# Kernel optimization log

Hardware: AMD Instinct MI355X
Metric: run time of the kernel (lower is better)

Reference implementation:

```python
import jax, jax.numpy as jnp
import numpy as np

B, S, D, H, E, F = 32, 196, 768, 12, 8, 3072  # batch, seq, d_model, heads, experts, ffn
DH = D // H
EPS = 1e-5


def setup_inputs() -> dict:
    key = jax.random.key(0)
    ks = jax.random.split(key, 16)
    n = lambda k, shape, s=0.02: (jax.random.normal(k, shape, dtype=jnp.float32) * s)
    return {
        "q": jax.random.normal(ks[0], (B, S, D), dtype=jnp.float32),
        "k": jax.random.normal(ks[1], (B, S, D), dtype=jnp.float32),
        "v": jax.random.normal(ks[2], (B, S, D), dtype=jnp.float32),
        "Wq": n(ks[3], (D, D)), "bq": jnp.zeros((D,), jnp.float32),
        "Wk": n(ks[4], (D, D)), "bk": jnp.zeros((D,), jnp.float32),
        "Wv": n(ks[5], (D, D)), "bv": jnp.zeros((D,), jnp.float32),
        "Wo": n(ks[6], (D, D)), "bo": jnp.zeros((D,), jnp.float32),
        "ln1_g": jnp.ones((D,), jnp.float32), "ln1_b": jnp.zeros((D,), jnp.float32),
        "ln2_g": jnp.ones((D,), jnp.float32), "ln2_b": jnp.zeros((D,), jnp.float32),
        "Wg": n(ks[7], (D, E)), "bg": jnp.zeros((E,), jnp.float32),
        "W1": n(ks[8], (E, D, F)), "b1": jnp.zeros((E, F), jnp.float32),
        "W2": n(ks[9], (E, F, D)), "b2": jnp.zeros((E, D), jnp.float32),
    }


def _layernorm(x, g, b):
    mu = jnp.mean(x, axis=-1, keepdims=True)
    var = jnp.mean(jnp.square(x - mu), axis=-1, keepdims=True)
    return (x - mu) * jax.lax.rsqrt(var + EPS) * g + b


def reference(q, k, v, Wq, bq, Wk, bk, Wv, bv, Wo, bo,
              ln1_g, ln1_b, ln2_g, ln2_b, Wg, bg, W1, b1, W2, b2):
    # --- multi-head attention (batch_first, scaled dot product) ---
    qh = (q @ Wq + bq).reshape(B, S, H, DH)
    kh = (k @ Wk + bk).reshape(B, S, H, DH)
    vh = (v @ Wv + bv).reshape(B, S, H, DH)
    scores = jnp.einsum('bqhd,bkhd->bhqk', qh, kh) / np.float32(np.sqrt(DH))
    attn = jax.nn.softmax(scores, axis=-1)
    ctx = jnp.einsum('bhqk,bkhd->bqhd', attn, vh).reshape(B, S, D)
    attn_out = ctx @ Wo + bo

    # --- residual + LN 1 ---
    x = _layernorm(q + attn_out, ln1_g, ln1_b)

    # --- MoE: per-token soft gating over per-expert FFNs ---
    gates = jax.nn.softmax(x @ Wg + bg, axis=-1)                 # [B,S,E]
    h = jax.nn.gelu(jnp.einsum('bsd,edf->bsef', x, W1) + b1,
                    approximate=False)                            # [B,S,E,F]
    y = jnp.einsum('bsef,efd->bsed', h, W2) + b2                 # [B,S,E,D]
    moe_out = jnp.einsum('bse,bsed->bsd', gates, y)              # [B,S,D]

    # --- residual + LN 2 ---
    return _layernorm(x + moe_out, ln2_g, ln2_b)
```

## Files before the change

kernel.cpp:

```cpp
#include <hip/hip_runtime.h>
#include <cmath>

#define B_  32
#define S_  196
#define D_  768
#define H_  12
#define E_  8
#define F_  3072
#define DH_ 64
#define T_  (B_ * S_)

typedef unsigned short ushort_t;
typedef short   s16x8   __attribute__((ext_vector_type(8)));
typedef __bf16  bf16x8_t __attribute__((ext_vector_type(8)));
typedef float   f32x4   __attribute__((ext_vector_type(4)));

struct ABFrag {
    unsigned int r[4];
    __device__ operator s16x8()    const { return __builtin_bit_cast(s16x8, *this); }
    __device__ operator bf16x8_t() const { return __builtin_bit_cast(bf16x8_t, *this); }
};

__device__ __forceinline__ ushort_t f2bf(float f) {
    unsigned int x = __float_as_uint(f);
    return (ushort_t)((x + 0x7fffu + ((x >> 16) & 1u)) >> 16);
}

__device__ __forceinline__ void glds16(const void* g, void* l) {
    __builtin_amdgcn_global_load_lds((const __attribute__((address_space(1))) void*)g,
                                     (__attribute__((address_space(3))) void*)l,
                                     16, 0, 0);
}

template<int EPI>
__global__ __launch_bounds__(256)
void gemm_bt(const ushort_t* __restrict__ A, const ushort_t* __restrict__ Bt,
             const float* __restrict__ bias,
             float* __restrict__ Cf, ushort_t* __restrict__ Cb,
             int M, int N, int K,
             const float* __restrict__ gates, int expert)
{
    __shared__ ushort_t Alds[128 * 32];
    __shared__ ushort_t Blds[128 * 32];

    const int tid = threadIdx.x;
    const int w  = tid >> 6, l = tid & 63;
    const int wr = w >> 1,  wc = w & 1;
    const int rg = l >> 4,  fr = l & 15;
    const int brow = blockIdx.y * 128;
    const int bcol = blockIdx.x * 128;

    const int srow = tid >> 2;
    const int scol = (tid & 3) << 3;
    const ushort_t* gA = A  + (size_t)(brow + srow) * K + scol;
    const ushort_t* gB = Bt + (size_t)(bcol + srow) * K + scol;
    ushort_t* lA = &Alds[w * 512];
    ushort_t* lB = &Blds[w * 512];

    f32x4 acc[4][4] = {};

    const int aoff = (wr * 64 + fr) * 32 + rg * 8;
    const int boff = (wc * 64 + fr) * 32 + rg * 8;

    for (int k0 = 0; k0 < K; k0 += 32) {
        if (k0) __syncthreads();
        glds16(gA,                  lA);
        glds16(gA + (size_t)64 * K, lA + 2048);
        glds16(gB,                  lB);
        glds16(gB + (size_t)64 * K, lB + 2048);
        gA += 32; gB += 32;
        __syncthreads();

        ABFrag af[4], bf[4];
        #pragma unroll
        for (int m = 0; m < 4; ++m) af[m] = *(const ABFrag*)&Alds[aoff + m * 512];
        #pragma unroll
        for (int n = 0; n < 4; ++n) bf[n] = *(const ABFrag*)&Blds[boff + n * 512];
        #pragma unroll
        for (int m = 0; m < 4; ++m)
            #pragma unroll
            for (int n = 0; n < 4; ++n)
                acc[m][n] = __builtin_amdgcn_mfma_f32_16x16x32_bf16(
                                af[m], bf[n], acc[m][n], 0, 0, 0);
    }

    #pragma unroll
    for (int m = 0; m < 4; ++m) {
        #pragma unroll
        for (int n = 0; n < 4; ++n) {
            const int col = bcol + wc * 64 + n * 16 + fr;
            const float bv = bias[col];
            #pragma unroll
            for (int j = 0; j < 4; ++j) {
                const int row = brow + wr * 64 + m * 16 + rg * 4 + j;
                float vv = acc[m][n][j] + bv;
                if (EPI == 0) {
                    Cf[(size_t)row * N + col] = vv;
                } else if (EPI == 1) {
                    vv = 0.5f * vv * (1.0f + erff(vv * 0.70710678118654752f));
                    Cb[(size_t)row * N + col] = f2bf(vv);
                } else {
                    Cf[(size_t)row * N + col] +=
                        gates[(size_t)row * E_ + expert] * vv;
                }
            }
        }
    }
}

__global__ __launch_bounds__(256)
void convert_bf16(const float* __restrict__ in, ushort_t* __restrict__ out)
{
    const int i = blockIdx.x * 256 + threadIdx.x;
    float4 v = ((const float4*)in)[i];
    ushort4 o;
    o.x = f2bf(v.x); o.y = f2bf(v.y); o.z = f2bf(v.z); o.w = f2bf(v.w);
    ((ushort4*)out)[i] = o;
}

__global__ __launch_bounds__(256)
void transpose_to_bf16(const float* __restrict__ in, ushort_t* __restrict__ out,
                       int R, int C)
{
    __shared__ float tile[64][65];
    const int bc = blockIdx.x * 64;
    const int br = blockIdx.y * 64;
    const int lr = threadIdx.x >> 4;
    const int lc = (threadIdx.x & 15) << 2;
    #pragma unroll
    for (int i = 0; i < 64; i += 16) {
        float4 v = *(const float4*)&in[(size_t)(br + lr + i) * C + bc + lc];
        tile[lr + i][lc + 0] = v.x; tile[lr + i][lc + 1] = v.y;
        tile[lr + i][lc + 2] = v.z; tile[lr + i][lc + 3] = v.w;
    }
    __syncthreads();
    #pragma unroll
    for (int i = 0; i < 64; i += 16) {
        const int orow = lr + i;
        ushort4 o;
        o.x = f2bf(tile[lc + 0][orow]);
        o.y = f2bf(tile[lc + 1][orow]);
        o.z = f2bf(tile[lc + 2][orow]);
        o.w = f2bf(tile[lc + 3][orow]);
        *(ushort4*)&out[(size_t)(bc + orow) * R + br + lc] = o;
    }
}

__global__ __launch_bounds__(256)
void attn_kernel(const float* __restrict__ qh, const float* __restrict__ kh,
                 const float* __restrict__ vh, float* __restrict__ ctx,
                 float* __restrict__ scratch)
{
    __shared__ float Ks[S_ * DH_];
    const int bh = blockIdx.x;
    const int b  = bh / H_;
    const int h  = bh % H_;
    const int tid = threadIdx.x;

    for (int idx = tid; idx < S_ * DH_; idx += 256) {
        const int s = idx >> 6, d = idx & 63;
        Ks[idx] = kh[((size_t)(b * S_ + s)) * D_ + h * DH_ + d];
    }
    __syncthreads();
    if (tid >= S_) return;

    float qf[DH_];
    const float* qrow = qh + ((size_t)(b * S_ + tid)) * D_ + h * DH_;
    #pragma unroll
    for (int d4 = 0; d4 < 16; ++d4) {
        float4 v4 = *(const float4*)(qrow + d4 * 4);
        qf[d4*4+0] = v4.x; qf[d4*4+1] = v4.y; qf[d4*4+2] = v4.z; qf[d4*4+3] = v4.w;
    }

    float* sc = scratch + (size_t)bh * (S_ * S_) + tid;
    float m = -1e30f;
    for (int k = 0; k < S_; ++k) {
        const float* kr = &Ks[k * DH_];
        float s0 = 0.f, s1 = 0.f, s2 = 0.f, s3 = 0.f;
        #pragma unroll
        for (int d = 0; d < DH_; d += 4) {
            s0 = fmaf(qf[d+0], kr[d+0], s0);
            s1 = fmaf(qf[d+1], kr[d+1], s1);
            s2 = fmaf(qf[d+2], kr[d+2], s2);
            s3 = fmaf(qf[d+3], kr[d+3], s3);
        }
        const float sv = (s0 + s1 + s2 + s3) * 0.125f;
        sc[(size_t)k * S_] = sv;
        m = fmaxf(m, sv);
    }
    float l = 0.f;
    for (int k = 0; k < S_; ++k) {
        const float p = expf(sc[(size_t)k * S_] - m);
        sc[(size_t)k * S_] = p;
        l += p;
    }
    float acc[DH_];
    #pragma unroll
    for (int d = 0; d < DH_; ++d) acc[d] = 0.f;
    const float* vbase = vh + ((size_t)b * S_) * D_ + h * DH_;
    for (int k = 0; k < S_; ++k) {
        const float p = sc[(size_t)k * S_];
        const float* vr = vbase + (size_t)k * D_;
        #pragma unroll
        for (int d4 = 0; d4 < 16; ++d4) {
            float4 v4 = *(const float4*)(vr + d4 * 4);
            acc[d4*4+0] = fmaf(p, v4.x, acc[d4*4+0]);
            acc[d4*4+1] = fmaf(p, v4.y, acc[d4*4+1]);
            acc[d4*4+2] = fmaf(p, v4.z, acc[d4*4+2]);
            acc[d4*4+3] = fmaf(p, v4.w, acc[d4*4+3]);
        }
    }
    const float inv = 1.f / l;
    float* crow = ctx + ((size_t)(b * S_ + tid)) * D_ + h * DH_;
    #pragma unroll
    for (int d = 0; d < DH_; ++d) crow[d] = acc[d] * inv;
}

__device__ __forceinline__ float block_sum(float v, float* red)
{
    __syncthreads();
    const int lane = threadIdx.x & 63;
    const int wid  = threadIdx.x >> 6;
    #pragma unroll
    for (int off = 32; off > 0; off >>= 1) v += __shfl_down(v, off);
    if (lane == 0) red[wid] = v;
    __syncthreads();
    return red[0] + red[1] + red[2] + red[3];
}

__global__ __launch_bounds__(256)
void ln_kernel(const float* __restrict__ a, const float* __restrict__ bres,
               const float* __restrict__ g, const float* __restrict__ beta,
               float* __restrict__ out)
{
    __shared__ float red[4];
    const int t   = blockIdx.x;
    const int tid = threadIdx.x;
    const float* ar = a    + (size_t)t * D_;
    const float* br = bres + (size_t)t * D_;

    float vals[3];
    float s = 0.f;
    #pragma unroll
    for (int i = 0; i < 3; ++i) {
        const int d = tid + i * 256;
        const float x = ar[d] + br[d];
        vals[i] = x;
        s += x;
    }
    s = block_sum(s, red);
    const float mu = s * (1.f / D_);
    float qv = 0.f;
    #pragma unroll
    for (int i = 0; i < 3; ++i) { const float dv = vals[i] - mu; qv += dv * dv; }
    qv = block_sum(qv, red);
    const float rstd = rsqrtf(qv * (1.f / D_) + 1e-5f);
    #pragma unroll
    for (int i = 0; i < 3; ++i) {
        const int d = tid + i * 256;
        out[(size_t)t * D_ + d] = (vals[i] - mu) * rstd * g[d] + beta[d];
    }
}

__global__ __launch_bounds__(256)
void gate_kernel(const float* __restrict__ x, const float* __restrict__ Wg,
                 const float* __restrict__ bg, float* __restrict__ gates)
{
    const int lane = threadIdx.x & 63;
    const int wid  = threadIdx.x >> 6;
    const int t = blockIdx.x * 4 + wid;
    const float* xr = x + (size_t)t * D_;

    float accv[E_];
    #pragma unroll
    for (int e = 0; e < E_; ++e) accv[e] = 0.f;
    for (int d = lane; d < D_; d += 64) {
        const float xv = xr[d];
        const float* wr = Wg + (size_t)d * E_;
        #pragma unroll
        for (int e = 0; e < E_; ++e) accv[e] = fmaf(xv, wr[e], accv[e]);
    }
    #pragma unroll
    for (int e = 0; e < E_; ++e) {
        #pragma unroll
        for (int off = 32; off > 0; off >>= 1)
            accv[e] += __shfl_down(accv[e], off);
    }
    if (lane == 0) {
        float mx = -1e30f;
        #pragma unroll
        for (int e = 0; e < E_; ++e) { accv[e] += bg[e]; mx = fmaxf(mx, accv[e]); }
        float l = 0.f;
        #pragma unroll
        for (int e = 0; e < E_; ++e) { const float p = expf(accv[e] - mx); accv[e] = p; l += p; }
        const float inv = 1.f / l;
        #pragma unroll
        for (int e = 0; e < E_; ++e) gates[(size_t)t * E_ + e] = accv[e] * inv;
    }
}

__global__ void zero_kernel(float* __restrict__ p, int n)
{
    const int i = blockIdx.x * blockDim.x + threadIdx.x;
    if (i < n) p[i] = 0.f;
}

extern "C" void kernel_launch(void* const* d_in, const int* in_sizes, int n_in,
                              void* d_out, int out_size, void* d_ws, size_t ws_size,
                              hipStream_t stream)
{
    const float* q    = (const float*)d_in[0];
    const float* k    = (const float*)d_in[1];
    const float* v    = (const float*)d_in[2];
    const float* Wq   = (const float*)d_in[3];
    const float* bq   = (const float*)d_in[4];
    const float* Wk   = (const float*)d_in[5];
    const float* bk   = (const float*)d_in[6];
    const float* Wv   = (const float*)d_in[7];
    const float* bv   = (const float*)d_in[8];
    const float* Wo   = (const float*)d_in[9];
    const float* bo   = (const float*)d_in[10];
    const float* ln1g = (const float*)d_in[11];
    const float* ln1b = (const float*)d_in[12];
    const float* ln2g = (const float*)d_in[13];
    const float* ln2b = (const float*)d_in[14];
    const float* Wg   = (const float*)d_in[15];
    const float* bg   = (const float*)d_in[16];
    const float* W1   = (const float*)d_in[17];
    const float* b1   = (const float*)d_in[18];
    const float* W2   = (const float*)d_in[19];
    const float* b2   = (const float*)d_in[20];
    float* out = (float*)d_out;
    float* ws  = (float*)d_ws;

    const size_t TD = (size_t)T_ * D_;
    const size_t SC = (size_t)B_ * H_ * S_ * S_;

    float* qh     = ws;
    float* kh     = ws + TD;
    float* vh     = ws + 2 * TD;
    float* ctx    = ws + 3 * TD;
    float* moe    = ws + 4 * TD;
    float* scores = ws + 4 * TD;
    ushort_t* bigu = (ushort_t*)(ws + 5 * TD);
    ushort_t* qb   = bigu;
    ushort_t* kb   = bigu + TD;
    ushort_t* vb   = bigu + 2 * TD;
    ushort_t* ctxb = bigu;
    ushort_t* hb   = bigu;
    ushort_t* xb   = (ushort_t*)vh;
    float* gates   = vh + TD / 2;
    float* attnout = qh;
    float* x       = kh;

    ushort_t* wqt = (ushort_t*)(ws + 4 * TD + SC);
    ushort_t* wkt = wqt + (size_t)D_ * D_;
    ushort_t* wvt = wkt + (size_t)D_ * D_;
    ushort_t* wot = wvt + (size_t)D_ * D_;
    ushort_t* w1t = wot + (size_t)D_ * D_;
    ushort_t* w2t = w1t + (size_t)F_ * D_;

    const dim3 blk(256);
    const dim3 gD(D_ / 128, T_ / 128);
    const dim3 gF(F_ / 128, T_ / 128);
    const int cgrid = (int)(TD / 1024);

    convert_bf16<<<cgrid, blk, 0, stream>>>(q, qb);
    convert_bf16<<<cgrid, blk, 0, stream>>>(k, kb);
    convert_bf16<<<cgrid, blk, 0, stream>>>(v, vb);
    transpose_to_bf16<<<dim3(D_/64, D_/64), blk, 0, stream>>>(Wq, wqt, D_, D_);
    transpose_to_bf16<<<dim3(D_/64, D_/64), blk, 0, stream>>>(Wk, wkt, D_, D_);
    transpose_to_bf16<<<dim3(D_/64, D_/64), blk, 0, stream>>>(Wv, wvt, D_, D_);
    transpose_to_bf16<<<dim3(D_/64, D_/64), blk, 0, stream>>>(Wo, wot, D_, D_);
    gemm_bt<0><<<gD, blk, 0, stream>>>(qb, wqt, bq, qh, nullptr, T_, D_, D_, nullptr, 0);
    gemm_bt<0><<<gD, blk, 0, stream>>>(kb, wkt, bk, kh, nullptr, T_, D_, D_, nullptr, 0);
    gemm_bt<0><<<gD, blk, 0, stream>>>(vb, wvt, bv, vh, nullptr, T_, D_, D_, nullptr, 0);

    attn_kernel<<<dim3(B_ * H_), blk, 0, stream>>>(qh, kh, vh, ctx, scores);

    convert_bf16<<<cgrid, blk, 0, stream>>>(ctx, ctxb);
    gemm_bt<0><<<gD, blk, 0, stream>>>(ctxb, wot, bo, attnout, nullptr, T_, D_, D_, nullptr, 0);
    ln_kernel<<<dim3(T_), blk, 0, stream>>>(q, attnout, ln1g, ln1b, x);

    gate_kernel<<<dim3(T_ / 4), blk, 0, stream>>>(x, Wg, bg, gates);
    convert_bf16<<<cgrid, blk, 0, stream>>>(x, xb);

    const int nmoe = T_ * D_;
    zero_kernel<<<dim3((nmoe + 255) / 256), blk, 0, stream>>>(moe, nmoe);
    for (int e = 0; e < E_; ++e) {
        transpose_to_bf16<<<dim3(F_/64, D_/64), blk, 0, stream>>>(
            W1 + (size_t)e * D_ * F_, w1t, D_, F_);
        transpose_to_bf16<<<dim3(D_/64, F_/64), blk, 0, stream>>>(
            W2 + (size_t)e * F_ * D_, w2t, F_, D_);
        gemm_bt<1><<<gF, blk, 0, stream>>>(xb, w1t, b1 + (size_t)e * F_,
                                           nullptr, hb, T_, F_, D_, nullptr, 0);
        gemm_bt<2><<<gD, blk, 0, stream>>>(hb, w2t, b2 + (size_t)e * D_,
                                           moe, nullptr, T_, D_, F_, gates, e);
    }

    ln_kernel<<<dim3(T_), blk, 0, stream>>>(x, moe, ln2g, ln2b, out);
}
```

Measured before the change: 1.711 ms.

## Fuse QKV GEMMs, online-softmax attention, split-K atomic W2 GEMM, fold zeroing into LN

Measured after the change: 1.900 ms. +11.0%, slower.

```diff
diff --git a/kernel.cpp b/kernel.cpp
--- a/kernel.cpp
+++ b/kernel.cpp
@@ -32,12 +32,18 @@
                                      16, 0, 0);
 }
 
+__device__ __forceinline__ void atomAddF(float* p, float v) {
+    __hip_atomic_fetch_add(p, v, __ATOMIC_RELAXED, __HIP_MEMORY_SCOPE_AGENT);
+}
+
 template<int EPI>
 __global__ __launch_bounds__(256)
-void gemm_bt(const ushort_t* __restrict__ A, const ushort_t* __restrict__ Bt,
+void gemm_bt(const ushort_t* __restrict__ A0, const ushort_t* __restrict__ A1,
+             const ushort_t* __restrict__ A2, const ushort_t* __restrict__ Bt,
              const float* __restrict__ bias,
-             float* __restrict__ Cf, ushort_t* __restrict__ Cb,
-             int M, int N, int K,
+             float* __restrict__ C0, float* __restrict__ C1,
+             float* __restrict__ C2, ushort_t* __restrict__ Cb,
+             int M, int N, int K, int lda, int ldb,
              const float* __restrict__ gates, int expert)
 {
     __shared__ ushort_t Alds[128 * 32];
@@ -49,59 +55,67 @@
     const int rg = l >> 4,  fr = l & 15;
     const int brow = blockIdx.y * 128;
     const int bcol = blockIdx.x * 128;
+    const int koff = blockIdx.z * K;
+
+    const int seg = (EPI == 3) ? (bcol / 768) : 0;
+    const ushort_t* A = (EPI == 3) ? (seg == 0 ? A0 : seg == 1 ? A1 : A2) : A0;
+    float* Cf         = (EPI == 3) ? (seg == 0 ? C0 : seg == 1 ? C1 : C2) : C0;
+    const int ldc     = (EPI == 3) ? 768 : N;
+    const int ccol0   = bcol - seg * 768;
 
     const int srow = tid >> 2;
     const int scol = (tid & 3) << 3;
-    const ushort_t* gA = A  + (size_t)(brow + srow) * K + scol;
-    const ushort_t* gB = Bt + (size_t)(bcol + srow) * K + scol;
+    const ushort_t* gA = A  + (size_t)(brow + srow) * lda + koff + scol;
+    const ushort_t* gB = Bt + (size_t)(bcol + srow) * ldb + koff + scol;
     ushort_t* lA = &Alds[w * 512];
     ushort_t* lB = &Blds[w * 512];
 
     f32x4 acc[4][4] = {};
-
     const int aoff = (wr * 64 + fr) * 32 + rg * 8;
     const int boff = (wc * 64 + fr) * 32 + rg * 8;
 
     for (int k0 = 0; k0 < K; k0 += 32) {
         if (k0) __syncthreads();
-        glds16(gA,                  lA);
-        glds16(gA + (size_t)64 * K, lA + 2048);
-        glds16(gB,                  lB);
-        glds16(gB + (size_t)64 * K, lB + 2048);
+        glds16(gA,                    lA);
+        glds16(gA + (size_t)64 * lda, lA + 2048);
+        glds16(gB,                    lB);
+        glds16(gB + (size_t)64 * ldb, lB + 2048);
         gA += 32; gB += 32;
         __syncthreads();
 
-        ABFrag af[4], bf[4];
-        #pragma unroll
-        for (int m = 0; m < 4; ++m) af[m] = *(const ABFrag*)&Alds[aoff + m * 512];
-        #pragma unroll
-        for (int n = 0; n < 4; ++n) bf[n] = *(const ABFrag*)&Blds[boff + n * 512];
+        ABFrag af[4], bfr[4];
+        #pragma unroll
+        for (int m = 0; m < 4; ++m) af[m]  = *(const ABFrag*)&Alds[aoff + m * 512];
+        #pragma unroll
+        for (int n = 0; n < 4; ++n) bfr[n] = *(const ABFrag*)&Blds[boff + n * 512];
         #pragma unroll
         for (int m = 0; m < 4; ++m)
             #pragma unroll
             for (int n = 0; n < 4; ++n)
                 acc[m][n] = __builtin_amdgcn_mfma_f32_16x16x32_bf16(
-                                af[m], bf[n], acc[m][n], 0, 0, 0);
+                                af[m], bfr[n], acc[m][n], 0, 0, 0);
     }
 
     #pragma unroll
     for (int m = 0; m < 4; ++m) {
         #pragma unroll
         for (int n = 0; n < 4; ++n) {
-            const int col = bcol + wc * 64 + n * 16 + fr;
-            const float bv = bias[col];
+            const int cg  = bcol + wc * 64 + n * 16 + fr;
+            const int col = ccol0 + wc * 64 + n * 16 + fr;
+            float bv = bias[cg];
+            if (EPI == 2 && blockIdx.z != 0) bv = 0.f;
             #pragma unroll
             for (int j = 0; j < 4; ++j) {
                 const int row = brow + wr * 64 + m * 16 + rg * 4 + j;
                 float vv = acc[m][n][j] + bv;
-                if (EPI == 0) {
-                    Cf[(size_t)row * N + col] = vv;
-                } else if (EPI == 1) {
+                if (EPI == 1) {
                     vv = 0.5f * vv * (1.0f + erff(vv * 0.70710678118654752f));
                     Cb[(size_t)row * N + col] = f2bf(vv);
+                } else if (EPI == 2) {
+                    atomAddF(&Cf[(size_t)row * ldc + col],
+                             gates[(size_t)row * E_ + expert] * vv);
                 } else {
-                    Cf[(size_t)row * N + col] +=
-                        gates[(size_t)row * E_ + expert] * vv;
+                    Cf[(size_t)row * ldc + col] = vv;
                 }
             }
         }
@@ -148,8 +162,7 @@
 
 __global__ __launch_bounds__(256)
 void attn_kernel(const float* __restrict__ qh, const float* __restrict__ kh,
-                 const float* __restrict__ vh, float* __restrict__ ctx,
-                 float* __restrict__ scratch)
+                 const float* __restrict__ vh, float* __restrict__ ctx)
 {
     __shared__ float Ks[S_ * DH_];
     const int bh = blockIdx.x;
@@ -157,9 +170,10 @@
     const int h  = bh % H_;
     const int tid = threadIdx.x;
 
-    for (int idx = tid; idx < S_ * DH_; idx += 256) {
-        const int s = idx >> 6, d = idx & 63;
-        Ks[idx] = kh[((size_t)(b * S_ + s)) * D_ + h * DH_ + d];
+    for (int i = tid; i < S_ * 16; i += 256) {
+        const int s = i >> 4, d4 = i & 15;
+        ((float4*)Ks)[s * 16 + d4] =
+            *(const float4*)&kh[((size_t)(b * S_ + s)) * D_ + h * DH_ + d4 * 4];
     }
     __syncthreads();
     if (tid >= S_) return;
@@ -167,13 +181,16 @@
     float qf[DH_];
     const float* qrow = qh + ((size_t)(b * S_ + tid)) * D_ + h * DH_;
     #pragma unroll
-    for (int d4 = 0; d4 < 16; ++d4) {
-        float4 v4 = *(const float4*)(qrow + d4 * 4);
-        qf[d4*4+0] = v4.x; qf[d4*4+1] = v4.y; qf[d4*4+2] = v4.z; qf[d4*4+3] = v4.w;
-    }
-
-    float* sc = scratch + (size_t)bh * (S_ * S_) + tid;
-    float m = -1e30f;
+    for (int d = 0; d < DH_; d += 4) {
+        float4 v4 = *(const float4*)(qrow + d);
+        qf[d+0] = v4.x * 0.125f; qf[d+1] = v4.y * 0.125f;
+        qf[d+2] = v4.z * 0.125f; qf[d+3] = v4.w * 0.125f;
+    }
+
+    float m = -1e30f, lsum = 0.f;
+    float acc[DH_] = {};
+    const float* vbase = vh + ((size_t)b * S_) * D_ + h * DH_;
+
     for (int k = 0; k < S_; ++k) {
         const float* kr = &Ks[k * DH_];
         float s0 = 0.f, s1 = 0.f, s2 = 0.f, s3 = 0.f;
@@ -184,33 +201,27 @@
             s2 = fmaf(qf[d+2], kr[d+2], s2);
             s3 = fmaf(qf[d+3], kr[d+3], s3);
         }
-        const float sv = (s0 + s1 + s2 + s3) * 0.125f;
-        sc[(size_t)k * S_] = sv;
-        m = fmaxf(m, sv);
-    }
-    float l = 0.f;
-    for (int k = 0; k < S_; ++k) {
-        const float p = expf(sc[(size_t)k * S_] - m);
-        sc[(size_t)k * S_] = p;
-        l += p;
-    }
-    float acc[DH_];
-    #pragma unroll
-    for (int d = 0; d < DH_; ++d) acc[d] = 0.f;
-    const float* vbase = vh + ((size_t)b * S_) * D_ + h * DH_;
-    for (int k = 0; k < S_; ++k) {
-        const float p = sc[(size_t)k * S_];
+        const float sv = (s0 + s1) + (s2 + s3);
+        if (sv > m) {
+            const float alpha = __expf(m - sv);
+            lsum *= alpha;
+            #pragma unroll
+            for (int d = 0; d < DH_; ++d) acc[d] *= alpha;
+            m = sv;
+        }
+        const float p = __expf(sv - m);
+        lsum += p;
         const float* vr = vbase + (size_t)k * D_;
         #pragma unroll
-        for (int d4 = 0; d4 < 16; ++d4) {
-            float4 v4 = *(const float4*)(vr + d4 * 4);
-            acc[d4*4+0] = fmaf(p, v4.x, acc[d4*4+0]);
-            acc[d4*4+1] = fmaf(p, v4.y, acc[d4*4+1]);
-            acc[d4*4+2] = fmaf(p, v4.z, acc[d4*4+2]);
-            acc[d4*4+3] = fmaf(p, v4.w, acc[d4*4+3]);
+        for (int d = 0; d < DH_; d += 4) {
+            float4 v4 = *(const float4*)(vr + d);
+            acc[d+0] = fmaf(p, v4.x, acc[d+0]);
+            acc[d+1] = fmaf(p, v4.y, acc[d+1]);
+            acc[d+2] = fmaf(p, v4.z, acc[d+2]);
+            acc[d+3] = fmaf(p, v4.w, acc[d+3]);
         }
     }
-    const float inv = 1.f / l;
+    const float inv = 1.f / lsum;
     float* crow = ctx + ((size_t)(b * S_ + tid)) * D_ + h * DH_;
     #pragma unroll
     for (int d = 0; d < DH_; ++d) crow[d] = acc[d] * inv;
@@ -231,7 +242,7 @@
 __global__ __launch_bounds__(256)
 void ln_kernel(const float* __restrict__ a, const float* __restrict__ bres,
                const float* __restrict__ g, const float* __restrict__ beta,
-               float* __restrict__ out)
+               float* __restrict__ out, float* __restrict__ zt)
 {
     __shared__ float red[4];
     const int t   = blockIdx.x;
@@ -247,6 +258,7 @@
         const float x = ar[d] + br[d];
         vals[i] = x;
         s += x;
+        if (zt) zt[(size_t)t * D_ + d] = 0.f;
     }
     s = block_sum(s, red);
     const float mu = s * (1.f / D_);
@@ -290,19 +302,22 @@
         float mx = -1e30f;
         #pragma unroll
         for (int e = 0; e < E_; ++e) { accv[e] += bg[e]; mx = fmaxf(mx, accv[e]); }
-        float l = 0.f;
-        #pragma unroll
-        for (int e = 0; e < E_; ++e) { const float p = expf(accv[e] - mx); accv[e] = p; l += p; }
-        const float inv = 1.f / l;
+        float lsum = 0.f;
+        #pragma unroll
+        for (int e = 0; e < E_; ++e) { const float p = expf(accv[e] - mx); accv[e] = p; lsum += p; }
+        const float inv = 1.f / lsum;
         #pragma unroll
         for (int e = 0; e < E_; ++e) gates[(size_t)t * E_ + e] = accv[e] * inv;
     }
 }
 
-__global__ void zero_kernel(float* __restrict__ p, int n)
-{
-    const int i = blockIdx.x * blockDim.x + threadIdx.x;
-    if (i < n) p[i] = 0.f;
+__global__ void concat3_kernel(const float* __restrict__ a, const float* __restrict__ b,
+                               const float* __restrict__ c, float* __restrict__ o)
+{
+    const int i = blockIdx.x * 256 + threadIdx.x;
+    if (i < 768)       o[i] = a[i];
+    else if (i < 1536) o[i] = b[i - 768];
+    else if (i < 2304) o[i] = c[i - 1536];
 }
 
 extern "C" void kernel_launch(void* const* d_in, const int* in_sizes, int n_in,
@@ -334,69 +349,72 @@
     float* ws  = (float*)d_ws;
 
     const size_t TD = (size_t)T_ * D_;
-    const size_t SC = (size_t)B_ * H_ * S_ * S_;
-
-    float* qh     = ws;
-    float* kh     = ws + TD;
-    float* vh     = ws + 2 * TD;
-    float* ctx    = ws + 3 * TD;
-    float* moe    = ws + 4 * TD;
-    float* scores = ws + 4 * TD;
-    ushort_t* bigu = (ushort_t*)(ws + 5 * TD);
-    ushort_t* qb   = bigu;
-    ushort_t* kb   = bigu + TD;
-    ushort_t* vb   = bigu + 2 * TD;
-    ushort_t* ctxb = bigu;
-    ushort_t* hb   = bigu;
-    ushort_t* xb   = (ushort_t*)vh;
-    float* gates   = vh + TD / 2;
+    const size_t DD = (size_t)D_ * D_;
+    const size_t DF = (size_t)D_ * F_;
+
+    float* qh      = ws;
+    float* x       = ws + TD;
+    float* kh      = x;
+    float* vh      = ws + 2 * TD;
+    float* ctx     = ws + 3 * TD;
+    float* moe     = ws + 4 * TD;
+    ushort_t* hb   = (ushort_t*)(ws + 2 * TD);
+    ushort_t* xb   = (ushort_t*)qh;
+    float* gates   = qh + TD / 2;
     float* attnout = qh;
-    float* x       = kh;
-
-    ushort_t* wqt = (ushort_t*)(ws + 4 * TD + SC);
-    ushort_t* wkt = wqt + (size_t)D_ * D_;
-    ushort_t* wvt = wkt + (size_t)D_ * D_;
-    ushort_t* wot = wvt + (size_t)D_ * D_;
-    ushort_t* w1t = wot + (size_t)D_ * D_;
-    ushort_t* w2t = w1t + (size_t)F_ * D_;
+
+    ushort_t* qb   = (ushort_t*)(ws + 5 * TD);
+    ushort_t* kb   = qb + TD;
+    ushort_t* vb   = kb + TD;
+    ushort_t* ctxb = qb;
+
+    ushort_t* wqkvt = (ushort_t*)(ws + 6 * TD + TD / 2);
+    ushort_t* wot   = wqkvt + 3 * DD;
+    float*    bcat  = (float*)(wot + DD);
+    ushort_t* w1t   = (ushort_t*)(bcat + 2304);
+    ushort_t* w2t   = w1t + DF;
 
     const dim3 blk(256);
-    const dim3 gD(D_ / 128, T_ / 128);
-    const dim3 gF(F_ / 128, T_ / 128);
-    const int cgrid = (int)(TD / 1024);
+    const int  cgrid = (int)(TD / 1024);
+
+    concat3_kernel<<<dim3(9), blk, 0, stream>>>(bq, bk, bv, bcat);
+    transpose_to_bf16<<<dim3(D_/64, D_/64), blk, 0, stream>>>(Wq, wqkvt,          D_, D_);
+    transpose_to_bf16<<<dim3(D_/64, D_/64), blk, 0, stream>>>(Wk, wqkvt + DD,     D_, D_);
+    transpose_to_bf16<<<dim3(D_/64, D_/64), blk, 0, stream>>>(Wv, wqkvt + 2 * DD, D_, D_);
+    transpose_to_bf16<<<dim3(D_/64, D_/64), blk, 0, stream>>>(Wo, wot,            D_, D_);
 
     convert_bf16<<<cgrid, blk, 0, stream>>>(q, qb);
     convert_bf16<<<cgrid, blk, 0, stream>>>(k, kb);
     convert_bf16<<<cgrid, blk, 0, stream>>>(v, vb);
-    transpose_to_bf16<<<dim3(D_/64, D_/64), blk, 0, stream>>>(Wq, wqt, D_, D_);
-    transpose_to_bf16<<<dim3(D_/64, D_/64), blk, 0, stream>>>(Wk, wkt, D_, D_);
-    transpose_to_bf16<<<dim3(D_/64, D_/64), blk, 0, stream>>>(Wv, wvt, D_, D_);
-    transpose_to_bf16<<<dim3(D_/64, D_/64), blk, 0, stream>>>(Wo, wot, D_, D_);
-    gemm_bt<0><<<gD, blk, 0, stream>>>(qb, wqt, bq, qh, nullptr, T_, D_, D_, nullptr, 0);
-    gemm_bt<0><<<gD, blk, 0, stream>>>(kb, wkt, bk, kh, nullptr, T_, D_, D_, nullptr, 0);
-    gemm_bt<0><<<gD, blk, 0, stream>>>(vb, wvt, bv, vh, nullptr, T_, D_, D_, nullptr, 0);
-
-    attn_kernel<<<dim3(B_ * H_), blk, 0, stream>>>(qh, kh, vh, ctx, scores);
+    gemm_bt<3><<<dim3(18, 49), blk, 0, stream>>>(qb, kb, vb, wqkvt, bcat,
+                                                 qh, kh, vh, nullptr,
+                                                 T_, 2304, D_, D_, D_, nullptr, 0);
+
+    attn_kernel<<<dim3(B_ * H_), blk, 0, stream>>>(qh, kh, vh, ctx);
 
     convert_bf16<<<cgrid, blk, 0, stream>>>(ctx, ctxb);
-    gemm_bt<0><<<gD, blk, 0, stream>>>(ctxb, wot, bo, attnout, nullptr, T_, D_, D_, nullptr, 0);
-    ln_kernel<<<dim3(T_), blk, 0, stream>>>(q, attnout, ln1g, ln1b, x);
+    gemm_bt<0><<<dim3(6, 49), blk, 0, stream>>>(ctxb, nullptr, nullptr, wot, bo,
+                                                attnout, nullptr, nullptr, nullptr,
+                                                T_, D_, D_, D_, D_, nullptr, 0);
+    ln_kernel<<<dim3(T_), blk, 0, stream>>>(q, attnout, ln1g, ln1b, x, moe);
 
     gate_kernel<<<dim3(T_ / 4), blk, 0, stream>>>(x, Wg, bg, gates);
     convert_bf16<<<cgrid, blk, 0, stream>>>(x, xb);
 
-    const int nmoe = T_ * D_;
-    zero_kernel<<<dim3((nmoe + 255) / 256), blk, 0, stream>>>(moe, nmoe);
     for (int e = 0; e < E_; ++e) {
         transpose_to_bf16<<<dim3(F_/64, D_/64), blk, 0, stream>>>(
-            W1 + (size_t)e * D_ * F_, w1t, D_, F_);
+            W1 + (size_t)e * DF, w1t, D_, F_);
         transpose_to_bf16<<<dim3(D_/64, F_/64), blk, 0, stream>>>(
-            W2 + (size_t)e * F_ * D_, w2t, F_, D_);
-        gemm_bt<1><<<gF, blk, 0, stream>>>(xb, w1t, b1 + (size_t)e * F_,
-                                           nullptr, hb, T_, F_, D_, nullptr, 0);
-        gemm_bt<2><<<gD, blk, 0, stream>>>(hb, w2t, b2 + (size_t)e * D_,
-                                           moe, nullptr, T_, D_, F_, gates, e);
-    }
-
-    ln_kernel<<<dim3(T_), blk, 0, stream>>>(x, moe, ln2g, ln2b, out);
-}
+            W2 + (size_t)e * DF, w2t, F_, D_);
+        gemm_bt<1><<<dim3(24, 49), blk, 0, stream>>>(xb, nullptr, nullptr, w1t,
+                                                     b1 + (size_t)e * F_,
+                                                     nullptr, nullptr, nullptr, hb,
+                                                     T_, F_, D_, D_, D_, nullptr, 0);
+        gemm_bt<2><<<dim3(6, 49, 4), blk, 0, stream>>>(hb, nullptr, nullptr, w2t,
+                                                       b2 + (size_t)e * D_,
+                                                       moe, nullptr, nullptr, nullptr,
+                                                       T_, D_, 768, F_, F_, gates, e);
+    }
+
+    ln_kernel<<<dim3(T_), blk, 0, stream>>>(x, moe, ln2g, ln2b, out, nullptr);
+}
```
